# Performance work log

Hardware: AMD Instinct MI355X
Metric: run time of the kernel (lower is better)

## Reference

```python
import jax, jax.numpy as jnp
import numpy as np

# Geometry constants (LinearProbeGeom)
N_DET = 128
N_T = 2048
DT_S = 2.5e-08        # 40 MHz sampling
PITCH_M = 3.0e-04
C_M_S = 1540.0
NX, NY = 256, 256
X0_M, DX_M = -0.0192, 1.5e-04
Y0_M, DY_M = 1.0e-03, 1.5e-04
ARRAY_X0_M, ARRAY_Y_M = -0.0192, 0.0
N_FFT = N_T  # fft_pad = 0
EPS = np.float32(np.finfo(np.float32).eps)


def _constants():
    freq = np.fft.rfftfreq(N_FFT, d=DT_S)
    omega = (2.0 * np.pi * freq).astype(np.float32)            # (F,)
    fw = np.ones_like(omega)
    if omega.size > 2:
        fw[1:-1] = 2.0
    if N_FFT % 2 == 0 and omega.size > 1:
        fw[-1] = 1.0
    kx = (2.0 * np.pi * np.fft.fftfreq(N_DET, d=PITCH_M)).astype(np.float32)  # (D,)
    xs = (X0_M + np.arange(NX) * DX_M - ARRAY_X0_M).astype(np.float32)        # (X,)
    ys = (Y0_M + np.arange(NY) * DY_M - ARRAY_Y_M).astype(np.float32)         # (Y,)
    # Hann apodization over detectors (buffer, non-trainable)
    apod = (0.5 - 0.5 * np.cos(2.0 * np.pi * np.arange(N_DET) / max(N_DET - 1, 1))).astype(np.float32)
    return (jnp.asarray(omega), jnp.asarray(fw), jnp.asarray(kx),
            jnp.asarray(xs), jnp.asarray(ys), jnp.asarray(apod))


def setup_inputs() -> dict:
    key = jax.random.key(0)
    sino = jax.random.normal(key, (8, 1, N_DET, N_T), dtype=jnp.float32)
    return {"sino": sino}


def reference(sino):
    omega, fw, kx, xs, ys, apod = _constants()
    B, C, D, T = sino.shape
    # per-(B,C) standardization over (det, time)
    mean = jnp.mean(sino, axis=(-1, -2), keepdims=True)
    sn = sino - mean
    var = jnp.mean(sn * sn, axis=(-1, -2), keepdims=True)
    sn = sn / jnp.sqrt(var + EPS)
    # time window is rectangular (window=None) -> identity
    sw = sn * apod[None, None, :, None]
    # 2D spectrum: rfft over time, fft over detectors
    spec = jnp.fft.rfft(sw, n=N_FFT, axis=-1)          # (B,C,D,F)
    spec = jnp.fft.fft(spec, axis=2)                   # (B,C,D,F)
    # Stolt dispersion: kz^2 = (w/c)^2 - kx^2, clamped
    kz_sq = (omega / C_M_S)[None, :] ** 2 - (kx ** 2)[:, None]   # (D,F)
    kz = jnp.sqrt(jnp.maximum(kz_sq, 0.0))
    prop_mask = (kz_sq > 0.0).astype(jnp.float32)
    # fold propagation mask and frequency weighting into the spectrum
    sf = spec * (prop_mask * fw[None, :])[None, None, :, :]      # (B,C,D,F) complex
    # per-depth phase shift and frequency reduction
    phase_y = jnp.exp(1j * kz[None, :, :] * ys[:, None, None])   # (Y,D,F) complex64
    band = jnp.einsum('bcdf,ydf->bcyd', sf, phase_y)             # (B,C,Y,D)
    # lateral inverse transform via explicit phase matrix
    phase_x = jnp.exp(1j * kx[:, None] * xs[None, :])            # (D,X)
    img = jnp.einsum('bcyd,dx->bcyx', band, phase_x)             # (B,C,Y,X)
    img_mag = jnp.abs(img)
    apod_sum = jnp.maximum(jnp.sum(apod), EPS)
    fw_sum = jnp.maximum(jnp.sum(fw), EPS)
    return img_mag / (apod_sum * fw_sum)
```

## Files before the change

### kernel.cpp

```cpp
#include <hip/hip_runtime.h>
#include <math.h>

#define NB 8
#define ND 128
#define NT 2048
#define NF 1025
#define NYY 256
#define NXX 256

#define SPEC_BYTES 8396800
#define BAND_PART_BYTES 2097152
#define BANDH_PART_BYTES 1048576
#define ROWSTAT_OFF 0
#define SPECT_OFF  8192
#define SF_OFF     (SPECT_OFF + SPEC_BYTES)
#define BAND_OFF   (SF_OFF + SPEC_BYTES)

__global__ __launch_bounds__(256) void fk_tfft(const float* __restrict__ sino,
                                               float2* __restrict__ specT,
                                               float2* __restrict__ rowstat) {
  const int row = blockIdx.x;
  const int d = row & (ND - 1);
  const int tid = threadIdx.x;
  __shared__ float2 bufA[1024];
  __shared__ float2 bufB[1024];
  __shared__ float2 wsum[4];
  const float ap = (float)(0.5 - 0.5 * cos(6.283185307179586 * (double)d / 127.0));
  const float2* in = (const float2*)(sino + (size_t)row * NT);
  float s = 0.f, q = 0.f;
  for (int i = tid; i < 1024; i += 256) {
    float2 v = in[i];
    s += v.x + v.y;
    q += v.x * v.x + v.y * v.y;
    bufA[i] = make_float2(v.x * ap, v.y * ap);
  }
  #pragma unroll
  for (int o = 32; o > 0; o >>= 1) {
    s += __shfl_down(s, o);
    q += __shfl_down(q, o);
  }
  if ((tid & 63) == 0) wsum[tid >> 6] = make_float2(s, q);
  __syncthreads();
  if (tid == 0) {
    rowstat[row] = make_float2(wsum[0].x + wsum[1].x + wsum[2].x + wsum[3].x,
                               wsum[0].y + wsum[1].y + wsum[2].y + wsum[3].y);
  }
  float2* src = bufA;
  float2* dst = bufB;
  for (int p = 1; p <= 512; p <<= 1) {
    #pragma unroll
    for (int it = 0; it < 2; ++it) {
      int i = tid + it * 256;
      int k = i & (p - 1);
      float2 u = src[i];
      float2 v = src[i + 512];
      float ang = -3.14159265358979323846f * ((float)k / (float)p);
      float sn, cs; __sincosf(ang, &sn, &cs);
      float2 vw = make_float2(v.x * cs - v.y * sn, v.x * sn + v.y * cs);
      int j = ((i - k) << 1) + k;
      dst[j]     = make_float2(u.x + vw.x, u.y + vw.y);
      dst[j + p] = make_float2(u.x - vw.x, u.y - vw.y);
    }
    __syncthreads();
    float2* t = src; src = dst; dst = t;
  }
  float2* out = specT + (size_t)row * NF;
  for (int k = tid; k < 1024; k += 256) {
    float2 zk = src[k];
    float2 zc = src[(1024 - k) & 1023]; zc.y = -zc.y;
    float2 xe = make_float2(0.5f * (zk.x + zc.x), 0.5f * (zk.y + zc.y));
    float ax = zk.x - zc.x, ay = zk.y - zc.y;
    float2 xo = make_float2(0.5f * ay, -0.5f * ax);
    float ang = -3.14159265358979323846f * ((float)k / 1024.0f);
    float sn, cs; __sincosf(ang, &sn, &cs);
    out[k] = make_float2(xe.x + cs * xo.x - sn * xo.y,
                         xe.y + cs * xo.y + sn * xo.x);
  }
  if (tid == 0) {
    float2 z0 = src[0];
    out[1024] = make_float2(z0.x - z0.y, 0.0f);
  }
}

__global__ __launch_bounds__(256) void fk_dfft(const float2* __restrict__ specT,
                                               float2* __restrict__ sf) {
  const int b = blockIdx.y;
  const int f0 = blockIdx.x * 4;
  const int sub = threadIdx.x >> 6;
  const int i = threadIdx.x & 63;
  const int f = f0 + sub;
  const bool valid = (f < NF);
  __shared__ float2 A[4][128];
  __shared__ float2 Bf[4][128];
  if (valid) {
    const float2* col = specT + ((size_t)b * ND) * NF + f;
    A[sub][i]      = col[(size_t)i * NF];
    A[sub][i + 64] = col[(size_t)(i + 64) * NF];
  }
  __syncthreads();
  float2 (*src)[128] = A;
  float2 (*dst)[128] = Bf;
  for (int p = 1; p <= 64; p <<= 1) {
    if (valid) {
      int k = i & (p - 1);
      float2 u = src[sub][i];
      float2 v = src[sub][i + 64];
      float ang = -3.14159265358979323846f * ((float)k / (float)p);
      float sn, cs; __sincosf(ang, &sn, &cs);
      float2 vw = make_float2(v.x * cs - v.y * sn, v.x * sn + v.y * cs);
      int j = ((i - k) << 1) + k;
      dst[sub][j]     = make_float2(u.x + vw.x, u.y + vw.y);
      dst[sub][j + p] = make_float2(u.x - vw.x, u.y - vw.y);
    }
    __syncthreads();
    float2 (*t)[128] = src; src = dst; dst = t;
  }
  if (valid) {
    const float fwv = (f == 0 || f == NF - 1) ? 1.0f : 2.0f;
    double freqd = (double)f / 5.12e-5;
    float omega = (float)(freqd * 6.283185307179586);
    float woc = omega / 1540.0f;
    float woc2 = __fmul_rn(woc, woc);
    #pragma unroll
    for (int h = 0; h < 2; ++h) {
      int kd = i + h * 64;
      int kt = kd < 64 ? kd : kd - 128;
      float kxv = (float)(6.283185307179586 * ((double)kt / 0.0384));
      float kzsq = __fsub_rn(woc2, __fmul_rn(kxv, kxv));
      float m = (kzsq > 0.0f) ? fwv : 0.0f;
      float2 v = src[sub][kd];
      sf[((size_t)(b * ND + kd)) * NF + f] = make_float2(v.x * m, v.y * m);
    }
  }
}

__device__ __forceinline__ unsigned int bf16rne(float x) {
  unsigned int u = __float_as_uint(x);
  return (u + 0x7fffu + ((u >> 16) & 1u)) >> 16;
}

__global__ __launch_bounds__(256, 3) void fk_band(const float2* __restrict__ sf,
                                                  unsigned int* __restrict__ bandh,
                                                  int flen_base, int fpad) {
  const int dblk = blockIdx.x;
  const int part = blockIdx.y;
  const int f0 = part * flen_base;
  const int flen = min(flen_base, NF - f0);
  const int tid = threadIdx.x;
  const int w = tid >> 6, l = tid & 63;
  const int d = dblk * 4 + w;

  extern __shared__ float lds[];
  float2* sfs = (float2*)lds;
  float4* kcs = (float4*)(lds + 64 * fpad);

  {
    const int row = tid >> 3;
    const int wr = row >> 3, br = row & 7;
    const int dr = dblk * 4 + wr;
    const float2* srcp = sf + ((size_t)(br * ND + dr)) * NF + f0;
    for (int ff = tid & 7; ff < fpad; ff += 8)
      sfs[row * fpad + ff] = (ff < flen) ? srcp[ff] : make_float2(0.f, 0.f);
  }
  for (int e = tid; e < 4 * fpad; e += 256) {
    const int wk = e / fpad, ff = e - wk * fpad;
    float kzv = 0.f;
    if (ff < flen) {
      int dk = dblk * 4 + wk;
      int kt = dk < 64 ? dk : dk - 128;
      float kxv = (float)(6.283185307179586 * ((double)kt / 0.0384));
      float kx2 = __fmul_rn(kxv, kxv);
      int f = f0 + ff;
      double freqd = (double)f / 5.12e-5;
      float omega = (float)(freqd * 6.283185307179586);
      float woc = omega / 1540.0f;
      float kzsq = __fsub_rn(__fmul_rn(woc, woc), kx2);
      kzv = (kzsq > 0.0f) ? sqrtf(kzsq) : 0.0f;
    }
    float sd, cd;
    __sincosf(kzv * 1.5e-4f, &sd, &cd);
    kcs[e] = make_float4(kzv, cd, sd, 0.f);
  }
  __syncthreads();

  const float y0 = (float)(1.0e-3 + (double)(4 * l) * 1.5e-4);

  float2 acc[8][4];
  #pragma unroll
  for (int b = 0; b < 8; ++b)
    #pragma unroll
    for (int i = 0; i < 4; ++i) acc[b][i] = make_float2(0.f, 0.f);

  const float4* kcw = kcs + w * fpad;
  const float2* rows = sfs + (w * 8) * fpad;

  #pragma unroll 2
  for (int ff = 0; ff < fpad; ++ff) {
    const float4 k4 = kcw[ff];
    float s0, c0;
    __sincosf(k4.x * y0, &s0, &c0);
    float2 ph[4];
    ph[0] = make_float2(c0, s0);
    #pragma unroll
    for (int i = 0; i < 3; ++i)
      ph[i + 1] = make_float2(ph[i].x * k4.y - ph[i].y * k4.z,
                              ph[i].x * k4.z + ph[i].y * k4.y);
    #pragma unroll
    for (int b = 0; b < 8; ++b) {
      float2 p = rows[b * fpad + ff];
      #pragma unroll
      for (int i = 0; i < 4; ++i) {
        acc[b][i].x = fmaf(p.x, ph[i].x, fmaf(-p.y, ph[i].y, acc[b][i].x));
        acc[b][i].y = fmaf(p.x, ph[i].y, fmaf( p.y, ph[i].x, acc[b][i].y));
      }
    }
  }

  unsigned int* outp = bandh + (size_t)part * (NB * ND * NYY);
  #pragma unroll
  for (int b = 0; b < 8; ++b) {
    uint4 pk;
    pk.x = bf16rne(acc[b][0].x) | (bf16rne(acc[b][0].y) << 16);
    pk.y = bf16rne(acc[b][1].x) | (bf16rne(acc[b][1].y) << 16);
    pk.z = bf16rne(acc[b][2].x) | (bf16rne(acc[b][2].y) << 16);
    pk.w = bf16rne(acc[b][3].x) | (bf16rne(acc[b][3].y) << 16);
    ((uint4*)(outp + ((size_t)(b * ND + d)) * NYY))[l] = pk;
  }
}

__global__ __launch_bounds__(256) void fk_sum(const unsigned int* __restrict__ bandh,
                                              float2* __restrict__ bandS, int nparts) {
  const int n = blockIdx.x * 256 + threadIdx.x;
  float sx = 0.f, sy = 0.f;
  for (int p = 0; p < nparts; ++p) {
    unsigned int u = bandh[(size_t)p * (NB * ND * NYY) + n];
    sx += __uint_as_float(u << 16);
    sy += __uint_as_float(u & 0xffff0000u);
  }
  bandS[n] = make_float2(sx, sy);
}

__global__ __launch_bounds__(256) void fk_img(const float2* __restrict__ bandS,
                                              const float2* __restrict__ rowstat,
                                              float* __restrict__ out, float inv_norm) {
  const int y0 = blockIdx.x * 2;
  const int b = blockIdx.y;
  const int tid = threadIdx.x;
  const int half = tid >> 7;
  const int t = tid & 127;
  __shared__ float2 A[2][256];
  __shared__ float2 Bb[2][256];
  __shared__ float2 spart[2];
  {
    float2 v = bandS[((size_t)(b * ND + t)) * NYY + (y0 + half)];
    A[half][t]       = (t < 64)  ? v : make_float2(0.f, 0.f);
    A[half][t + 128] = (t >= 64) ? v : make_float2(0.f, 0.f);
  }
  {
    float2 myrs = make_float2(0.f, 0.f);
    if (tid < 128) myrs = rowstat[b * ND + tid];
    float s = myrs.x, q = myrs.y;
    #pragma unroll
    for (int o = 32; o > 0; o >>= 1) {
      s += __shfl_down(s, o);
      q += __shfl_down(q, o);
    }
    if (tid < 128 && (tid & 63) == 0) spart[tid >> 6] = make_float2(s, q);
  }
  __syncthreads();
  const float nInv = 1.0f / 262144.0f;
  float ssum = spart[0].x + spart[1].x;
  float qsum = spart[0].y + spart[1].y;
  float mean = ssum * nInv;
  float var = qsum * nInv - mean * mean;
  float scl = 1.0f / sqrtf(var + 1.1920928955078125e-7f);

  float2 (*src)[256] = A;
  float2 (*dst)[256] = Bb;
  for (int p = 1; p <= 128; p <<= 1) {
    int i = t;
    int k = i & (p - 1);
    float2 u = src[half][i];
    float2 v = src[half][i + 128];
    float ang = 3.14159265358979323846f * ((float)k / (float)p);
    float sn, cs; __sincosf(ang, &sn, &cs);
    float2 vw = make_float2(v.x * cs - v.y * sn, v.x * sn + v.y * cs);
    int j = ((i - k) << 1) + k;
    dst[half][j]     = make_float2(u.x + vw.x, u.y + vw.y);
    dst[half][j + p] = make_float2(u.x - vw.x, u.y - vw.y);
    __syncthreads();
    float2 (*tt)[256] = src; src = dst; dst = tt;
  }
  float2 r0 = src[0][tid];
  float2 r1 = src[1][tid];
  out[((size_t)b * NYY + y0)     * NXX + tid] = sqrtf(r0.x * r0.x + r0.y * r0.y) * scl * inv_norm;
  out[((size_t)b * NYY + y0 + 1) * NXX + tid] = sqrtf(r1.x * r1.x + r1.y * r1.y) * scl * inv_norm;
}

extern "C" void kernel_launch(void* const* d_in, const int* in_sizes, int n_in,
                              void* d_out, int out_size, void* d_ws, size_t ws_size,
                              hipStream_t stream) {
  const float* sino = (const float*)d_in[0];
  float* out = (float*)d_out;
  char* ws = (char*)d_ws;

  float2*       rowstat = (float2*)(ws + ROWSTAT_OFF);
  float2*       specT   = (float2*)(ws + SPECT_OFF);
  float2*       sf      = (float2*)(ws + SF_OFF);
  unsigned int* bandh   = (unsigned int*)(ws + BAND_OFF);

  int FPART = 8;
  if (ws_size >= (size_t)BAND_OFF + 24u * BANDH_PART_BYTES + BAND_PART_BYTES) FPART = 24;
  const int flen_base = (NF + FPART - 1) / FPART;
  const int fpad = (flen_base + 1) & ~1;
  const size_t band_lds = (size_t)fpad * 320;
  float2* bandS = (float2*)(ws + BAND_OFF + (size_t)FPART * BANDH_PART_BYTES);

  double apod_sum = 0.0;
  for (int n = 0; n < ND; ++n) apod_sum += 0.5 - 0.5 * cos(6.283185307179586 * (double)n / 127.0);
  const float inv_norm = (float)(1.0 / (apod_sum * 2048.0));

  fk_tfft<<<NB * ND, 256, 0, stream>>>(sino, specT, rowstat);
  fk_dfft<<<dim3((NF + 3) / 4, NB), 256, 0, stream>>>(specT, sf);
  fk_band<<<dim3(32, FPART), 256, band_lds, stream>>>(sf, bandh, flen_base, fpad);
  fk_sum <<<NB * ND * NYY / 256, 256, 0, stream>>>(bandh, bandS, FPART);
  fk_img <<<dim3(NYY / 2, NB), 256, 0, stream>>>(bandS, rowstat, out, inv_norm);
}
```

Before: 76.48 us.

## Compute depth-phase band reduction with bf16 MFMA instead of scalar FMAs

Adds a band kernel that casts the per-depth phase-weighted frequency reduction as a bf16 matrix multiply on MFMA 16x16x32 instructions. Phase factors are built in registers by complex rotation across depth tiles, and spectrum values are packed as bf16 real and imaginary operand pairs. This replaces the scalar FMA inner loop that reads from shared memory. In exchange, both phase and spectrum inputs are quantised to bf16, which costs accuracy, and the original kernel is kept as a fallback when the workspace is small.

```diff
diff --git a/kernel.cpp b/kernel.cpp
--- a/kernel.cpp
+++ b/kernel.cpp
@@ -1,4 +1,5 @@
 #include <hip/hip_runtime.h>
+#include <hip/hip_bf16.h>
 #include <math.h>
 
 #define NB 8
@@ -15,6 +16,16 @@
 #define SPECT_OFF  8192
 #define SF_OFF     (SPECT_OFF + SPEC_BYTES)
 #define BAND_OFF   (SF_OFF + SPEC_BYTES)
+
+typedef short bf16x8 __attribute__((ext_vector_type(8)));
+typedef float f32x4 __attribute__((ext_vector_type(4)));
+
+__device__ __forceinline__ unsigned pk2bf(float lo, float hi) {
+  __hip_bfloat162 h = __float22bfloat162_rn(make_float2(lo, hi));
+  unsigned u;
+  __builtin_memcpy(&u, &h, 4);
+  return u;
+}
 
 __global__ __launch_bounds__(256) void fk_tfft(const float* __restrict__ sino,
                                                float2* __restrict__ specT,
@@ -139,6 +150,103 @@
   return (u + 0x7fffu + ((u >> 16) & 1u)) >> 16;
 }
 
+__global__ __launch_bounds__(256, 3) void fk_band_mfma(const float2* __restrict__ sf,
+                                                       unsigned int* __restrict__ bandh,
+                                                       int flen_base) {
+  const int dblk = blockIdx.x;
+  const int part = blockIdx.y;
+  const int f0 = part * flen_base;
+  const int flen = min(flen_base, NF - f0);
+  const int tid = threadIdx.x;
+  const int lane = tid & 63;
+  const int d = dblk * 4 + (tid >> 6);
+  const int col = lane & 15;
+  const int grp = lane >> 4;
+
+  float kzv[3][4];
+  bf16x8 bfr[3], bfi[3];
+  #pragma unroll
+  for (int kt = 0; kt < 3; ++kt) {
+    union { unsigned u[4]; bf16x8 v; } ur, ui;
+    #pragma unroll
+    for (int c = 0; c < 4; ++c) {
+      const int fl = kt * 16 + grp * 4 + c;
+      float kv = 0.f;
+      float2 s = make_float2(0.f, 0.f);
+      if (fl < flen) {
+        const int fg = f0 + fl;
+        int ktd = d < 64 ? d : d - 128;
+        float kxv = (float)(6.283185307179586 * ((double)ktd / 0.0384));
+        float kx2 = __fmul_rn(kxv, kxv);
+        double freqd = (double)fg / 5.12e-5;
+        float omega = (float)(freqd * 6.283185307179586);
+        float woc = omega / 1540.0f;
+        float kzsq = __fsub_rn(__fmul_rn(woc, woc), kx2);
+        kv = (kzsq > 0.0f) ? sqrtf(kzsq) : 0.0f;
+        if (col < 8) s = sf[((size_t)(col * ND + d)) * NF + fg];
+      }
+      kzv[kt][c] = kv;
+      ur.u[c] = pk2bf(s.x, -s.y);
+      ui.u[c] = pk2bf(s.y,  s.x);
+    }
+    bfr[kt] = ur.v;
+    bfi[kt] = ui.v;
+  }
+
+  const float stepf = 2.4e-3f;
+  const int arow = lane & 15;
+  const f32x4 zz = {0.f, 0.f, 0.f, 0.f};
+
+  #pragma unroll
+  for (int h = 0; h < 2; ++h) {
+    f32x4 accre[8], accim[8];
+    #pragma unroll
+    for (int m = 0; m < 8; ++m) { accre[m] = zz; accim[m] = zz; }
+    const float yv0 = (float)(1.0e-3 + (double)(h * 128 + arow) * 1.5e-4);
+    #pragma unroll
+    for (int kt = 0; kt < 3; ++kt) {
+      float2 cur[4], stp[4];
+      #pragma unroll
+      for (int c = 0; c < 4; ++c) {
+        float sn, cs;
+        __sincosf(kzv[kt][c] * yv0, &sn, &cs);
+        cur[c] = make_float2(cs, sn);
+        __sincosf(kzv[kt][c] * stepf, &sn, &cs);
+        stp[c] = make_float2(cs, sn);
+      }
+      #pragma unroll
+      for (int m = 0; m < 8; ++m) {
+        union { unsigned u[4]; bf16x8 v; } ua;
+        #pragma unroll
+        for (int c = 0; c < 4; ++c) ua.u[c] = pk2bf(cur[c].x, cur[c].y);
+        accre[m] = __builtin_amdgcn_mfma_f32_16x16x32_bf16(ua.v, bfr[kt], accre[m], 0, 0, 0);
+        accim[m] = __builtin_amdgcn_mfma_f32_16x16x32_bf16(ua.v, bfi[kt], accim[m], 0, 0, 0);
+        #pragma unroll
+        for (int c = 0; c < 4; ++c) {
+          float2 nc;
+          nc.x = cur[c].x * stp[c].x - cur[c].y * stp[c].y;
+          nc.y = cur[c].x * stp[c].y + cur[c].y * stp[c].x;
+          cur[c] = nc;
+        }
+      }
+    }
+    if (col < 8) {
+      unsigned int* outp = bandh + (size_t)part * (NB * ND * NYY)
+                         + ((size_t)(col * ND + d)) * NYY;
+      #pragma unroll
+      for (int m = 0; m < 8; ++m) {
+        const int y0 = h * 128 + m * 16 + grp * 4;
+        uint4 pk;
+        pk.x = pk2bf(accre[m][0], accim[m][0]);
+        pk.y = pk2bf(accre[m][1], accim[m][1]);
+        pk.z = pk2bf(accre[m][2], accim[m][2]);
+        pk.w = pk2bf(accre[m][3], accim[m][3]);
+        *(uint4*)(outp + y0) = pk;
+      }
+    }
+  }
+}
+
 __global__ __launch_bounds__(256, 3) void fk_band(const float2* __restrict__ sf,
                                                   unsigned int* __restrict__ bandh,
                                                   int flen_base, int fpad) {
@@ -149,11 +257,9 @@
   const int tid = threadIdx.x;
   const int w = tid >> 6, l = tid & 63;
   const int d = dblk * 4 + w;
-
   extern __shared__ float lds[];
   float2* sfs = (float2*)lds;
   float4* kcs = (float4*)(lds + 64 * fpad);
-
   {
     const int row = tid >> 3;
     const int wr = row >> 3, br = row & 7;
@@ -182,18 +288,14 @@
     kcs[e] = make_float4(kzv, cd, sd, 0.f);
   }
   __syncthreads();
-
   const float y0 = (float)(1.0e-3 + (double)(4 * l) * 1.5e-4);
-
   float2 acc[8][4];
   #pragma unroll
   for (int b = 0; b < 8; ++b)
     #pragma unroll
     for (int i = 0; i < 4; ++i) acc[b][i] = make_float2(0.f, 0.f);
-
   const float4* kcw = kcs + w * fpad;
   const float2* rows = sfs + (w * 8) * fpad;
-
   #pragma unroll 2
   for (int ff = 0; ff < fpad; ++ff) {
     const float4 k4 = kcw[ff];
@@ -215,7 +317,6 @@
       }
     }
   }
-
   unsigned int* outp = bandh + (size_t)part * (NB * ND * NYY);
   #pragma unroll
   for (int b = 0; b < 8; ++b) {
@@ -309,20 +410,28 @@
   float2*       sf      = (float2*)(ws + SF_OFF);
   unsigned int* bandh   = (unsigned int*)(ws + BAND_OFF);
 
-  int FPART = 8;
-  if (ws_size >= (size_t)BAND_OFF + 24u * BANDH_PART_BYTES + BAND_PART_BYTES) FPART = 24;
-  const int flen_base = (NF + FPART - 1) / FPART;
-  const int fpad = (flen_base + 1) & ~1;
-  const size_t band_lds = (size_t)fpad * 320;
-  float2* bandS = (float2*)(ws + BAND_OFF + (size_t)FPART * BANDH_PART_BYTES);
-
   double apod_sum = 0.0;
   for (int n = 0; n < ND; ++n) apod_sum += 0.5 - 0.5 * cos(6.283185307179586 * (double)n / 127.0);
   const float inv_norm = (float)(1.0 / (apod_sum * 2048.0));
 
   fk_tfft<<<NB * ND, 256, 0, stream>>>(sino, specT, rowstat);
   fk_dfft<<<dim3((NF + 3) / 4, NB), 256, 0, stream>>>(specT, sf);
-  fk_band<<<dim3(32, FPART), 256, band_lds, stream>>>(sf, bandh, flen_base, fpad);
-  fk_sum <<<NB * ND * NYY / 256, 256, 0, stream>>>(bandh, bandS, FPART);
-  fk_img <<<dim3(NYY / 2, NB), 256, 0, stream>>>(bandS, rowstat, out, inv_norm);
-}
+
+  if (ws_size >= (size_t)BAND_OFF + 24u * BANDH_PART_BYTES + BAND_PART_BYTES) {
+    const int FPART = 24;
+    const int flen_base = (NF + FPART - 1) / FPART;
+    float2* bandS = (float2*)(ws + BAND_OFF + (size_t)FPART * BANDH_PART_BYTES);
+    fk_band_mfma<<<dim3(32, FPART), 256, 0, stream>>>(sf, bandh, flen_base);
+    fk_sum<<<NB * ND * NYY / 256, 256, 0, stream>>>(bandh, bandS, FPART);
+    fk_img<<<dim3(NYY / 2, NB), 256, 0, stream>>>(bandS, rowstat, out, inv_norm);
+  } else {
+    const int FPART = 8;
+    const int flen_base = (NF + FPART - 1) / FPART;
+    const int fpad = (flen_base + 1) & ~1;
+    const size_t band_lds = (size_t)fpad * 320;
+    float2* bandS = (float2*)(ws + BAND_OFF + (size_t)FPART * BANDH_PART_BYTES);
+    fk_band<<<dim3(32, FPART), 256, band_lds, stream>>>(sf, bandh, flen_base, fpad);
+    fk_sum<<<NB * ND * NYY / 256, 256, 0, stream>>>(bandh, bandS, FPART);
+    fk_img<<<dim3(NYY / 2, NB), 256, 0, stream>>>(bandS, rowstat, out, inv_norm);
+  }
+}
```

New measurement: 63.24 us. 17.3% less time.
